# Kernel tuning notes

Measured on AMD Instinct MI355X. Metric: run time of the kernel, lower is better.

## Reference

```python
import jax, jax.numpy as jnp
import numpy as np

B, N, D, H = 8, 1024, 256, 4  # batch, seq, input_dim==output_dim, heads
EPS = 1e-6


def _ln(h, gamma, beta):
    mu = jnp.mean(h, axis=-1, keepdims=True)
    var = jnp.mean(jnp.square(h - mu), axis=-1, keepdims=True)
    return (h - mu) * jax.lax.rsqrt(var + EPS) * gamma + beta


def setup_inputs() -> dict:
    key = jax.random.key(0)
    ks = jax.random.split(key, 8)
    x = jax.random.normal(ks[0], (B, N, D), dtype=jnp.float32)
    mask = jax.random.randint(ks[1], (B, N), 0, 2, dtype=jnp.int32)
    wq = jax.random.normal(ks[2], (H, D, D), dtype=jnp.float32) * 0.05
    wk = jax.random.normal(ks[3], (H, D, D), dtype=jnp.float32) * 0.05
    wv = jax.random.normal(ks[4], (H, D, D), dtype=jnp.float32) * 0.05
    wg = jax.random.uniform(ks[5], (H, D, D), dtype=jnp.float32, minval=-0.05, maxval=0.05)
    out_w = jax.random.normal(ks[6], (D * H, D), dtype=jnp.float32) * 0.05
    out_b = jnp.zeros((D,), dtype=jnp.float32)
    ln_g = jnp.ones((D,), jnp.float32); ln_b = jnp.zeros((D,), jnp.float32)
    lnr_g = jnp.ones((D,), jnp.float32); lnr_b = jnp.zeros((D,), jnp.float32)
    lno_g = jnp.ones((D,), jnp.float32); lno_b = jnp.zeros((D,), jnp.float32)
    return dict(x=x, mask=mask, wq=wq, wk=wk, wv=wv, wg=wg, out_w=out_w, out_b=out_b,
                ln_g=ln_g, ln_b=ln_b, lnr_g=lnr_g, lnr_b=lnr_b, lno_g=lno_g, lno_b=lno_b)


def reference(x, mask, wq, wk, wv, wg, out_w, out_b, ln_g, ln_b, lnr_g, lnr_b, lno_g, lno_b):
    m = mask.astype(jnp.float32)              # (B,N)
    scale = 1.0 / jnp.sqrt(jnp.float32(D))
    x_norm = _ln(x, ln_g, ln_b)               # (B,N,D)
    q = jnp.einsum('bnd,hde->hbne', x_norm, wq)
    k = jnp.einsum('bmd,hde->hbme', x_norm, wk)
    v = jnp.einsum('bmd,hde->hbme', x_norm, wv)
    att = jnp.einsum('hbne,hbme->hbnm', q, k) * scale  # (H,B,N,N)
    amask = m[:, :, None] * m[:, None, :]              # (B,N,N) outer-product mask
    att = att + (1.0 - amask)[None] * (-1e9)           # additive mask
    att = jax.nn.softmax(att, axis=-1) * amask[None]   # multiplicative mask
    out = jnp.einsum('hbnm,hbme->hbne', att, v)        # (H,B,N,D)
    gate = jax.nn.sigmoid(jnp.einsum('bnd,hde->hbne', x_norm, wg))
    out = out * gate
    out = out + x[None]                                # resnet per head
    out = _ln(out, lnr_g, lnr_b)
    out = jnp.transpose(out, (1, 2, 3, 0)).reshape(x.shape[0], x.shape[1], D * H)
    out = out @ out_w + out_b                          # (B,N,D)
    out = out + x                                      # resnet
    out = _ln(out, lno_g, lno_b)
    out = out * m[..., None]
    return out
```

## Files before the change

kernel.cpp:

```cpp
#include <hip/hip_runtime.h>
#include <hip/hip_bf16.h>

#define Bb 8
#define Nn 1024
#define Dd 256
#define Hh 4
#define ROWS 8192
#define EPSf 1e-6f

typedef __bf16 bf16t;
typedef bf16t bf16x8 __attribute__((ext_vector_type(8)));
typedef float f32x4 __attribute__((ext_vector_type(4)));

#define MFMA(a, b, c) __builtin_amdgcn_mfma_f32_16x16x32_bf16((a), (b), (c), 0, 0, 0)
#define GLB_U32(p) ((const __attribute__((address_space(1))) unsigned int*)(p))
#define LDS_U32(p) ((__attribute__((address_space(3))) unsigned int*)(p))

__device__ __forceinline__ bf16x8 load8(const bf16t* p) { return *(const bf16x8*)p; }

__device__ __forceinline__ float ldin(const void* p, size_t i, int flag) {
  return flag ? (float)((const bf16t*)p)[i] : ((const float*)p)[i];
}

__global__ void k_detect(const unsigned int* __restrict__ xw, int* __restrict__ flag) {
  int lane = threadIdx.x;
  int cnt = 0;
  for (int i = lane; i < 4096; i += 64) {
    unsigned int b1 = (xw[i] >> 8) & 0x7F;
    if (b1 >= 0x3B && b1 <= 0x43) cnt++;
  }
#pragma unroll
  for (int off = 32; off > 0; off >>= 1) cnt += __shfl_xor(cnt, off);
  if (lane == 0) *flag = (cnt > 2048) ? 1 : 0;
}

__global__ void k_prep(const void* p0, const void* p1, const void* p2, const void* p3,
                       const void* p4, const void* p5, const void* p6,
                       float* __restrict__ pf, const int* __restrict__ flagp) {
  int flag = *flagp;
  const void* ps[7] = {p0, p1, p2, p3, p4, p5, p6};
  int j = blockIdx.x, i = threadIdx.x;
  pf[j * 256 + i] = ldin(ps[j], i, flag);
}

__global__ __launch_bounds__(256) void k_ln(const void* __restrict__ x,
                                            const float* __restrict__ pf,
                                            bf16t* __restrict__ xn,
                                            float* __restrict__ xf,
                                            const int* __restrict__ flagp) {
  int flag = *flagp;
  int row = blockIdx.x * 4 + (threadIdx.x >> 6);
  int lane = threadIdx.x & 63;
  size_t base = (size_t)row * Dd;
  float v[4]; float s = 0.f, s2 = 0.f;
#pragma unroll
  for (int i = 0; i < 4; ++i) {
    v[i] = ldin(x, base + lane * 4 + i, flag);
    s += v[i]; s2 += v[i] * v[i];
  }
#pragma unroll
  for (int off = 32; off > 0; off >>= 1) {
    s += __shfl_xor(s, off);
    s2 += __shfl_xor(s2, off);
  }
  float mu = s * (1.f / Dd);
  float var = fmaxf(s2 * (1.f / Dd) - mu * mu, 0.f);
  float rs = rsqrtf(var + EPSf);
#pragma unroll
  for (int i = 0; i < 4; ++i) {
    int d = lane * 4 + i;
    xf[base + d] = v[i];
    xn[base + d] = (bf16t)((v[i] - mu) * rs * pf[d] + pf[256 + d]);
  }
}

__global__ __launch_bounds__(256) void k_trall(
    const void* __restrict__ wq, const void* __restrict__ wk,
    const void* __restrict__ wv, const void* __restrict__ wg,
    const void* __restrict__ ow, bf16t* __restrict__ wtAll,
    bf16t* __restrict__ owT, const int* __restrict__ flagp) {
  int flag = *flagp;
  __shared__ bf16t tile[32][33];
  int t = blockIdx.x;
  const void* in; bf16t* out; int R, C; size_t ibase;
  int r0, c0;
  if (t < 1024) {
    int w = t >> 8, z = (t >> 6) & 3, t64 = t & 63;
    r0 = (t64 >> 3) * 32; c0 = (t64 & 7) * 32;
    const void* srcs[4] = {wq, wk, wv, wg};
    const int tslot[4] = {0, 1, 3, 2};
    in = srcs[w]; ibase = (size_t)z * 65536;
    out = wtAll + (size_t)(tslot[w] * 4 + z) * 65536;
    R = 256; C = 256;
  } else {
    int t2 = t - 1024;
    c0 = (t2 & 7) * 32; r0 = (t2 >> 3) * 32;
    in = ow; ibase = 0; out = owT; R = 1024; C = 256;
  }
  int tx = threadIdx.x & 31, ty = threadIdx.x >> 5;
#pragma unroll
  for (int i = 0; i < 32; i += 8)
    tile[ty + i][tx] = (bf16t)ldin(in, ibase + (size_t)(r0 + ty + i) * C + c0 + tx, flag);
  __syncthreads();
#pragma unroll
  for (int i = 0; i < 32; i += 8)
    out[(size_t)(c0 + ty + i) * R + r0 + tx] = tile[tx][ty + i];
}

__global__ __launch_bounds__(256) void k_qkvg(
    const bf16t* __restrict__ xn, const bf16t* __restrict__ wtAll,
    bf16t* __restrict__ q, bf16t* __restrict__ kk,
    bf16t* __restrict__ g, bf16t* __restrict__ vt) {
  const int wave = threadIdx.x >> 6, lane = threadIdx.x & 63;
  const int quad = lane >> 4, l16 = lane & 15;
  const int mi = blockIdx.x, ni = blockIdx.y;
  const int row0 = mi * 128;
  const int instw = ni >> 1, colIn = (ni & 1) * 128;
  const int tt = instw >> 2, h = instw & 3;
  const int rB = (wave >> 1) * 64, cB = (wave & 1) * 64;

  const bf16t* Bsrc = wtAll + (size_t)instw * 65536 + (size_t)colIn * 256;

  __shared__ bf16t aT[4096];
  __shared__ bf16t bT[4096];
  __shared__ bf16t ct[128 * 136];

  f32x4 acc[4][4];
#pragma unroll
  for (int i = 0; i < 4; ++i)
#pragma unroll
    for (int j = 0; j < 4; ++j) acc[i][j] = (f32x4){0.f, 0.f, 0.f, 0.f};

  for (int k0 = 0; k0 < 256; k0 += 32) {
#pragma unroll
    for (int ii = 0; ii < 2; ++ii) {
      int inst = wave * 2 + ii;
      int idx = inst * 64 + lane;
      int r = idx >> 2, cp = idx & 3;
      int c = cp ^ ((r >> 1) & 3);
      __builtin_amdgcn_global_load_lds(GLB_U32(xn + (size_t)(row0 + r) * 256 + k0 + c * 8),
                                       LDS_U32(aT + inst * 512), 16, 0, 0);
    }
#pragma unroll
    for (int ii = 0; ii < 2; ++ii) {
      int inst = wave * 2 + ii;
      int idx = inst * 64 + lane;
      int r = idx >> 2, cp = idx & 3;
      int c = cp ^ ((r >> 1) & 3);
      __builtin_amdgcn_global_load_lds(GLB_U32(Bsrc + (size_t)r * 256 + k0 + c * 8),
                                       LDS_U32(bT + inst * 512), 16, 0, 0);
    }
    __syncthreads();

    bf16x8 aF[4], bF[4];
#pragma unroll
    for (int i = 0; i < 4; ++i) {
      int r = rB + i * 16 + l16;
      aF[i] = *(const bf16x8*)&aT[(r * 4 + (quad ^ ((r >> 1) & 3))) * 8];
    }
#pragma unroll
    for (int j = 0; j < 4; ++j) {
      int r = cB + j * 16 + l16;
      bF[j] = *(const bf16x8*)&bT[(r * 4 + (quad ^ ((r >> 1) & 3))) * 8];
    }
#pragma unroll
    for (int i = 0; i < 4; ++i)
#pragma unroll
      for (int j = 0; j < 4; ++j)
        acc[i][j] = MFMA(aF[i], bF[j], acc[i][j]);
    __syncthreads();
  }

  const bool tr = (tt == 3);
#pragma unroll
  for (int i = 0; i < 4; ++i)
#pragma unroll
    for (int j = 0; j < 4; ++j)
#pragma unroll
      for (int r = 0; r < 4; ++r) {
        int rl = rB + i * 16 + quad * 4 + r, cl = cB + j * 16 + l16;
        if (tr) ct[cl * 136 + rl] = (bf16t)acc[i][j][r];
        else    ct[rl * 136 + cl] = (bf16t)acc[i][j][r];
      }
  __syncthreads();
  if (!tr) {
    bf16t* base = (tt == 0 ? q : (tt == 1 ? kk : g)) +
                  (size_t)h * ROWS * Dd + (size_t)row0 * Dd + colIn;
#pragma unroll
    for (int it = 0; it < 8; ++it) {
      int rl = it * 16 + (threadIdx.x >> 4), c8 = (threadIdx.x & 15) * 8;
      *(bf16x8*)(base + (size_t)rl * Dd + c8) = *(const bf16x8*)&ct[rl * 136 + c8];
    }
  } else {
    int bb = row0 >> 10, n0 = row0 & 1023;
    bf16t* base = vt + (size_t)(h * Bb + bb) * Dd * Nn + (size_t)colIn * Nn + n0;
#pragma unroll
    for (int it = 0; it < 8; ++it) {
      int el = it * 16 + (threadIdx.x >> 4), c8 = (threadIdx.x & 15) * 8;
      *(bf16x8*)(base + (size_t)el * Nn + c8) = *(const bf16x8*)&ct[el * 136 + c8];
    }
  }
}

__global__ __launch_bounds__(256) void k_flash(
    const bf16t* __restrict__ qb, const bf16t* __restrict__ kb,
    const bf16t* __restrict__ vtb, const bf16t* __restrict__ gb,
    const float* __restrict__ xf, const int* __restrict__ mask,
    const float* __restrict__ pf, bf16t* __restrict__ tout) {
  const int wave = threadIdx.x >> 6, lane = threadIdx.x & 63;
  const int quad = lane >> 4, l16 = lane & 15;
  const int lin = blockIdx.x + 16 * blockIdx.y + 128 * blockIdx.z;
  const int hbp = lin & 31, tile = lin >> 5;
  const int b = hbp & 7, h = hbp >> 3;
  const int qrow0 = tile * 64 + wave * 16;

  const bf16t* Q = qb + (size_t)hbp * Nn * Dd;
  const bf16t* K = kb + (size_t)hbp * Nn * Dd;
  const bf16t* V = vtb + (size_t)hbp * Dd * Nn;
  const bf16t* G = gb + (size_t)hbp * Nn * Dd;

  __shared__ bf16t klds[32 * 256];
  __shared__ bf16t vlds[2][256 * 32];
  __shared__ bf16t pl[4 * 16 * 32];
  __shared__ float cm[Nn];

#define SWZ(row_) (((row_) & 3) ^ (((row_) >> 2) & 3))
#define STAGE_K(kt_) do {                                                      \
    _Pragma("unroll") for (int i_ = 0; i_ < 4; ++i_) {                         \
      int inst_ = wave * 4 + i_; int qq_ = inst_ * 64 + lane;                  \
      int r_ = qq_ >> 5, cp_ = qq_ & 31; int c_ = cp_ ^ (r_ & 15);             \
      __builtin_amdgcn_global_load_lds(                                        \
          GLB_U32(K + (size_t)((kt_) + r_) * Dd + c_ * 8),                     \
          LDS_U32(klds + inst_ * 512), 16, 0, 0); } } while (0)
#define STAGE_V(kt_, buf_) do {                                                \
    _Pragma("unroll") for (int i_ = 0; i_ < 4; ++i_) {                         \
      int inst_ = wave * 4 + i_; int qq_ = inst_ * 64 + lane;                  \
      int r_ = qq_ >> 2, cp_ = qq_ & 3; int c_ = cp_ ^ SWZ(r_);                \
      __builtin_amdgcn_global_load_lds(                                        \
          GLB_U32(V + (size_t)r_ * Nn + (kt_) + c_ * 8),                       \
          LDS_U32(vlds[buf_] + inst_ * 512), 16, 0, 0); } } while (0)

  STAGE_V(0, 0);
  STAGE_K(0);
  for (int i = threadIdx.x; i < Nn; i += 256) cm[i] = (float)mask[b * Nn + i];

  bf16x8 aq[8];
#pragma unroll
  for (int k8 = 0; k8 < 8; ++k8)
    aq[k8] = load8(Q + (size_t)(qrow0 + l16) * Dd + k8 * 32 + quad * 8);

  f32x4 oacc[16];
#pragma unroll
  for (int j = 0; j < 16; ++j) oacc[j] = (f32x4){0.f, 0.f, 0.f, 0.f};
  float lpart[4] = {0.f, 0.f, 0.f, 0.f};

  const float scale = 0.0625f;

  for (int kt = 0; kt < Nn; kt += 32) {
    const int vcur = (kt >> 5) & 1;
    __syncthreads();
    if (kt + 32 < Nn) STAGE_V(kt + 32, vcur ^ 1);

    f32x4 sacc[2];
    sacc[0] = (f32x4){0.f, 0.f, 0.f, 0.f};
    sacc[1] = (f32x4){0.f, 0.f, 0.f, 0.f};
#pragma unroll
    for (int k8 = 0; k8 < 8; ++k8)
#pragma unroll
      for (int j = 0; j < 2; ++j) {
        bf16x8 bk = *(const bf16x8*)&klds[((j * 16 + l16) * 32 + ((k8 * 4 + quad) ^ l16)) * 8];
        sacc[j] = MFMA(aq[k8], bk, sacc[j]);
      }

    float cmv0 = cm[kt + l16], cmv1 = cm[kt + 16 + l16];
#pragma unroll
    for (int j = 0; j < 2; ++j) {
      float cmv = j ? cmv1 : cmv0;
#pragma unroll
      for (int r = 0; r < 4; ++r) {
        float e = (cmv != 0.f) ? __expf(sacc[j][r] * scale) : 0.f;
        lpart[r] += e;
        int prow = quad * 4 + r;
        pl[wave * 512 + (prow * 4 + ((j * 2 + (l16 >> 3)) ^ SWZ(prow))) * 8 + (l16 & 7)] = (bf16t)e;
      }
    }

    __builtin_amdgcn_s_barrier();
    if (kt + 32 < Nn) STAGE_K(kt + 32);

    bf16x8 ap = *(const bf16x8*)&pl[wave * 512 + (l16 * 4 + (quad ^ SWZ(l16))) * 8];
#pragma unroll
    for (int j = 0; j < 16; ++j) {
      int e = j * 16 + l16;
      bf16x8 bv = *(const bf16x8*)&vlds[vcur][(e * 4 + (quad ^ SWZ(e))) * 8];
      oacc[j] = MFMA(ap, bv, oacc[j]);
    }
  }

#pragma unroll
  for (int r = 0; r < 4; ++r)
#pragma unroll
    for (int off = 1; off < 16; off <<= 1)
      lpart[r] += __shfl_xor(lpart[r], off);

  float inv[4];
#pragma unroll
  for (int r = 0; r < 4; ++r) {
    float rmv = cm[qrow0 + quad * 4 + r];
    inv[r] = (rmv != 0.f && lpart[r] > 1e-20f) ? 1.f / lpart[r] : 0.f;
  }
  float ps[4] = {0.f, 0.f, 0.f, 0.f}, pq[4] = {0.f, 0.f, 0.f, 0.f};
#pragma unroll
  for (int j = 0; j < 16; ++j) {
    int e = j * 16 + l16;
#pragma unroll
    for (int r = 0; r < 4; ++r) {
      int n = qrow0 + quad * 4 + r;
      float gv = (float)G[(size_t)n * Dd + e];
      float xv = xf[(size_t)(b * Nn + n) * Dd + e];
      float o = oacc[j][r] * inv[r] * (1.f / (1.f + __expf(-gv))) + xv;
      oacc[j][r] = o;
      ps[r] += o; pq[r] += o * o;
    }
  }
#pragma unroll
  for (int r = 0; r < 4; ++r) {
#pragma unroll
    for (int off = 1; off < 16; off <<= 1) {
      ps[r] += __shfl_xor(ps[r], off);
      pq[r] += __shfl_xor(pq[r], off);
    }
    float mu = ps[r] * (1.f / Dd);
    float rs = rsqrtf(fmaxf(pq[r] * (1.f / Dd) - mu * mu, 0.f) + EPSf);
    ps[r] = mu; pq[r] = rs;
  }
#pragma unroll
  for (int j = 0; j < 16; ++j) {
    int e = j * 16 + l16;
    float lg = pf[2 * 256 + e], lb = pf[3 * 256 + e];
#pragma unroll
    for (int r = 0; r < 4; ++r) {
      int n = qrow0 + quad * 4 + r;
      tout[((size_t)(b * Nn + n) * Dd + e) * Hh + h] =
          (bf16t)((oacc[j][r] - ps[r]) * pq[r] * lg + lb);
    }
  }
#undef STAGE_K
#undef STAGE_V
#undef SWZ
}

__global__ __launch_bounds__(256) void k_out(
    const bf16t* __restrict__ t, const bf16t* __restrict__ owT,
    const float* __restrict__ xf, const int* __restrict__ mask,
    const float* __restrict__ pf, void* __restrict__ outp,
    const int* __restrict__ flagp) {
  const int flag = *flagp;
  const int wave = threadIdx.x >> 6, lane = threadIdx.x & 63;
  const int quad = lane >> 4, l16 = lane & 15;
  const int row0 = blockIdx.x * 16;

  f32x4 acc[4];
#pragma unroll
  for (int j = 0; j < 4; ++j) acc[j] = (f32x4){0.f, 0.f, 0.f, 0.f};
  for (int k0 = 0; k0 < 1024; k0 += 32) {
    bf16x8 a = load8(t + (size_t)(row0 + l16) * 1024 + k0 + quad * 8);
#pragma unroll
    for (int j = 0; j < 4; ++j) {
      bf16x8 bb = load8(owT + (size_t)(wave * 64 + j * 16 + l16) * 1024 + k0 + quad * 8);
      acc[j] = MFMA(a, bb, acc[j]);
    }
  }
  __shared__ float redS[4][16], redQ[4][16];
  float ps[4] = {0.f, 0.f, 0.f, 0.f}, pq[4] = {0.f, 0.f, 0.f, 0.f};
#pragma unroll
  for (int j = 0; j < 4; ++j) {
    int e = wave * 64 + j * 16 + l16;
    float bias = pf[6 * 256 + e];
#pragma unroll
    for (int r = 0; r < 4; ++r) {
      int rr = row0 + quad * 4 + r;
      float o = acc[j][r] + bias + xf[(size_t)rr * Dd + e];
      acc[j][r] = o;
      ps[r] += o; pq[r] += o * o;
    }
  }
#pragma unroll
  for (int r = 0; r < 4; ++r) {
#pragma unroll
    for (int off = 1; off < 16; off <<= 1) {
      ps[r] += __shfl_xor(ps[r], off);
      pq[r] += __shfl_xor(pq[r], off);
    }
    if (l16 == 0) { redS[wave][quad * 4 + r] = ps[r]; redQ[wave][quad * 4 + r] = pq[r]; }
  }
  __syncthreads();
  float mu[4], rs[4], mk[4];
#pragma unroll
  for (int r = 0; r < 4; ++r) {
    int rl = quad * 4 + r;
    float ts = redS[0][rl] + redS[1][rl] + redS[2][rl] + redS[3][rl];
    float tq = redQ[0][rl] + redQ[1][rl] + redQ[2][rl] + redQ[3][rl];
    float m_ = ts * (1.f / Dd);
    mu[r] = m_;
    rs[r] = rsqrtf(fmaxf(tq * (1.f / Dd) - m_ * m_, 0.f) + EPSf);
    mk[r] = (float)mask[row0 + rl];
  }
#pragma unroll
  for (int j = 0; j < 4; ++j) {
    int e = wave * 64 + j * 16 + l16;
    float lg = pf[4 * 256 + e], lb = pf[5 * 256 + e];
#pragma unroll
    for (int r = 0; r < 4; ++r) {
      int rr = row0 + quad * 4 + r;
      float o = ((acc[j][r] - mu[r]) * rs[r] * lg + lb) * mk[r];
      size_t idx = (size_t)rr * Dd + e;
      if (flag) ((bf16t*)outp)[idx] = (bf16t)o;
      else      ((float*)outp)[idx] = o;
    }
  }
}

extern "C" void kernel_launch(void* const* d_in, const int* in_sizes, int n_in,
                              void* d_out, int out_size, void* d_ws, size_t ws_size,
                              hipStream_t stream) {
  const void* x    = d_in[0];
  const int*  mask = (const int*)d_in[1];
  const void* wq   = d_in[2];
  const void* wk   = d_in[3];
  const void* wv   = d_in[4];
  const void* wg   = d_in[5];
  const void* ow   = d_in[6];
  const void* ob   = d_in[7];
  const void* lng  = d_in[8];
  const void* lnb  = d_in[9];
  const void* lnrg = d_in[10];
  const void* lnrb = d_in[11];
  const void* lnog = d_in[12];
  const void* lnob = d_in[13];

  char* w = (char*)d_ws;
  int*   flag  = (int*)w;
  float* pf    = (float*)(w + 256);
  w += 8192;
  float* xf    = (float*)w; w += (size_t)ROWS * Dd * 4;
  bf16t* xn    = (bf16t*)w; w += (size_t)ROWS * Dd * 2;
  bf16t* wtAll = (bf16t*)w; w += (size_t)16 * Dd * Dd * 2;
  bf16t* owT   = (bf16t*)w; w += (size_t)Dd * 1024 * 2;
  bf16t* tb    = (bf16t*)w; w += (size_t)ROWS * 1024 * 2;
  bf16t* qb    = (bf16t*)w; w += (size_t)Hh * ROWS * Dd * 2;
  bf16t* kb    = (bf16t*)w; w += (size_t)Hh * ROWS * Dd * 2;
  bf16t* gb    = (bf16t*)w; w += (size_t)Hh * ROWS * Dd * 2;
  bf16t* vtb   = (bf16t*)w; w += (size_t)Hh * ROWS * Dd * 2;

  dim3 blk(256);
  k_detect<<<dim3(1), dim3(64), 0, stream>>>((const unsigned int*)x, flag);
  k_prep<<<dim3(7), blk, 0, stream>>>(lng, lnb, lnrg, lnrb, lnog, lnob, ob, pf, flag);
  k_ln<<<dim3(ROWS / 4), blk, 0, stream>>>(x, pf, xn, xf, flag);
  k_trall<<<dim3(1280), blk, 0, stream>>>(wq, wk, wv, wg, ow, wtAll, owT, flag);
  k_qkvg<<<dim3(64, 32), blk, 0, stream>>>(xn, wtAll, qb, kb, gb, vtb);
  k_flash<<<dim3(16, 8, 4), blk, 0, stream>>>(qb, kb, vtb, gb, xf, mask, pf, tb);
  k_out<<<dim3(512), blk, 0, stream>>>(tb, owT, xf, mask, pf, d_out, flag);
}
```

Measured before the change: 243.2 us.

## Fuse prep kernels into one launch, drop xf copy, stage k_out GEMM via LDS

Merges the dtype-detect, parameter-prep, input layernorm and weight-transpose kernels into a single block-partitioned launch, with each block re-detecting the dtype flag locally from a smaller sample. Stops materializing an fp32 copy of x; the flash and output kernels read the original input through the dtype-aware loader instead. k_out now stages its A and B tiles into swizzled LDS with async global-to-LDS loads rather than loading them per lane from global memory. This removes launch overhead and one full-size write, at the cost of redundant per-block detection and extra barriers in the output GEMM loop.

```diff
diff --git a/kernel.cpp b/kernel.cpp
--- a/kernel.cpp
+++ b/kernel.cpp
@@ -22,89 +22,93 @@
   return flag ? (float)((const bf16t*)p)[i] : ((const float*)p)[i];
 }
 
-__global__ void k_detect(const unsigned int* __restrict__ xw, int* __restrict__ flag) {
-  int lane = threadIdx.x;
-  int cnt = 0;
-  for (int i = lane; i < 4096; i += 64) {
-    unsigned int b1 = (xw[i] >> 8) & 0x7F;
-    if (b1 >= 0x3B && b1 <= 0x43) cnt++;
-  }
-#pragma unroll
-  for (int off = 32; off > 0; off >>= 1) cnt += __shfl_xor(cnt, off);
-  if (lane == 0) *flag = (cnt > 2048) ? 1 : 0;
-}
-
-__global__ void k_prep(const void* p0, const void* p1, const void* p2, const void* p3,
-                       const void* p4, const void* p5, const void* p6,
-                       float* __restrict__ pf, const int* __restrict__ flagp) {
-  int flag = *flagp;
-  const void* ps[7] = {p0, p1, p2, p3, p4, p5, p6};
-  int j = blockIdx.x, i = threadIdx.x;
-  pf[j * 256 + i] = ldin(ps[j], i, flag);
-}
-
-__global__ __launch_bounds__(256) void k_ln(const void* __restrict__ x,
-                                            const float* __restrict__ pf,
-                                            bf16t* __restrict__ xn,
-                                            float* __restrict__ xf,
-                                            const int* __restrict__ flagp) {
-  int flag = *flagp;
-  int row = blockIdx.x * 4 + (threadIdx.x >> 6);
-  int lane = threadIdx.x & 63;
-  size_t base = (size_t)row * Dd;
-  float v[4]; float s = 0.f, s2 = 0.f;
-#pragma unroll
-  for (int i = 0; i < 4; ++i) {
-    v[i] = ldin(x, base + lane * 4 + i, flag);
-    s += v[i]; s2 += v[i] * v[i];
-  }
-#pragma unroll
-  for (int off = 32; off > 0; off >>= 1) {
-    s += __shfl_xor(s, off);
-    s2 += __shfl_xor(s2, off);
-  }
-  float mu = s * (1.f / Dd);
-  float var = fmaxf(s2 * (1.f / Dd) - mu * mu, 0.f);
-  float rs = rsqrtf(var + EPSf);
-#pragma unroll
-  for (int i = 0; i < 4; ++i) {
-    int d = lane * 4 + i;
-    xf[base + d] = v[i];
-    xn[base + d] = (bf16t)((v[i] - mu) * rs * pf[d] + pf[256 + d]);
-  }
-}
-
-__global__ __launch_bounds__(256) void k_trall(
+__global__ __launch_bounds__(256) void k_prepall(
+    const void* __restrict__ x,
     const void* __restrict__ wq, const void* __restrict__ wk,
     const void* __restrict__ wv, const void* __restrict__ wg,
-    const void* __restrict__ ow, bf16t* __restrict__ wtAll,
-    bf16t* __restrict__ owT, const int* __restrict__ flagp) {
-  int flag = *flagp;
-  __shared__ bf16t tile[32][33];
-  int t = blockIdx.x;
-  const void* in; bf16t* out; int R, C; size_t ibase;
-  int r0, c0;
-  if (t < 1024) {
-    int w = t >> 8, z = (t >> 6) & 3, t64 = t & 63;
-    r0 = (t64 >> 3) * 32; c0 = (t64 & 7) * 32;
-    const void* srcs[4] = {wq, wk, wv, wg};
-    const int tslot[4] = {0, 1, 3, 2};
-    in = srcs[w]; ibase = (size_t)z * 65536;
-    out = wtAll + (size_t)(tslot[w] * 4 + z) * 65536;
-    R = 256; C = 256;
+    const void* __restrict__ ow,
+    const void* __restrict__ lng, const void* __restrict__ lnb,
+    const void* __restrict__ lnrg, const void* __restrict__ lnrb,
+    const void* __restrict__ lnog, const void* __restrict__ lnob,
+    const void* __restrict__ ob,
+    bf16t* __restrict__ xn, bf16t* __restrict__ wtAll,
+    bf16t* __restrict__ owT, float* __restrict__ pf, int* __restrict__ flagOut) {
+  __shared__ int sflag;
+  {
+    if (threadIdx.x < 64) {
+      int lane = threadIdx.x;
+      int cnt = 0;
+      const unsigned int* xw = (const unsigned int*)x;
+#pragma unroll
+      for (int i = 0; i < 4; ++i) {
+        unsigned int b1 = (xw[lane * 4 + i] >> 8) & 0x7F;
+        if (b1 >= 0x3B && b1 <= 0x43) cnt++;
+      }
+#pragma unroll
+      for (int off = 32; off > 0; off >>= 1) cnt += __shfl_xor(cnt, off);
+      if (lane == 0) sflag = (cnt > 128) ? 1 : 0;
+    }
+    __syncthreads();
+  }
+  const int flag = sflag;
+  const int bid = blockIdx.x;
+
+  if (bid < 2048) {
+    int row = bid * 4 + (threadIdx.x >> 6);
+    int lane = threadIdx.x & 63;
+    size_t base = (size_t)row * Dd;
+    float v[4]; float s = 0.f, s2 = 0.f;
+#pragma unroll
+    for (int i = 0; i < 4; ++i) {
+      v[i] = ldin(x, base + lane * 4 + i, flag);
+      s += v[i]; s2 += v[i] * v[i];
+    }
+#pragma unroll
+    for (int off = 32; off > 0; off >>= 1) {
+      s += __shfl_xor(s, off);
+      s2 += __shfl_xor(s2, off);
+    }
+    float mu = s * (1.f / Dd);
+    float var = fmaxf(s2 * (1.f / Dd) - mu * mu, 0.f);
+    float rs = rsqrtf(var + EPSf);
+#pragma unroll
+    for (int i = 0; i < 4; ++i) {
+      int d = lane * 4 + i;
+      xn[base + d] = (bf16t)((v[i] - mu) * rs * ldin(lng, d, flag) + ldin(lnb, d, flag));
+    }
+  } else if (bid < 3328) {
+    __shared__ bf16t tile[32][33];
+    int t = bid - 2048;
+    const void* in; bf16t* out; int R, C; size_t ibase;
+    int r0, c0;
+    if (t < 1024) {
+      int w = t >> 8, z = (t >> 6) & 3, t64 = t & 63;
+      r0 = (t64 >> 3) * 32; c0 = (t64 & 7) * 32;
+      const void* srcs[4] = {wq, wk, wv, wg};
+      const int tslot[4] = {0, 1, 3, 2};
+      in = srcs[w]; ibase = (size_t)z * 65536;
+      out = wtAll + (size_t)(tslot[w] * 4 + z) * 65536;
+      R = 256; C = 256;
+    } else {
+      int t2 = t - 1024;
+      c0 = (t2 & 7) * 32; r0 = (t2 >> 3) * 32;
+      in = ow; ibase = 0; out = owT; R = 1024; C = 256;
+    }
+    int tx = threadIdx.x & 31, ty = threadIdx.x >> 5;
+#pragma unroll
+    for (int i = 0; i < 32; i += 8)
+      tile[ty + i][tx] = (bf16t)ldin(in, ibase + (size_t)(r0 + ty + i) * C + c0 + tx, flag);
+    __syncthreads();
+#pragma unroll
+    for (int i = 0; i < 32; i += 8)
+      out[(size_t)(c0 + ty + i) * R + r0 + tx] = tile[tx][ty + i];
   } else {
-    int t2 = t - 1024;
-    c0 = (t2 & 7) * 32; r0 = (t2 >> 3) * 32;
-    in = ow; ibase = 0; out = owT; R = 1024; C = 256;
-  }
-  int tx = threadIdx.x & 31, ty = threadIdx.x >> 5;
-#pragma unroll
-  for (int i = 0; i < 32; i += 8)
-    tile[ty + i][tx] = (bf16t)ldin(in, ibase + (size_t)(r0 + ty + i) * C + c0 + tx, flag);
-  __syncthreads();
-#pragma unroll
-  for (int i = 0; i < 32; i += 8)
-    out[(size_t)(c0 + ty + i) * R + r0 + tx] = tile[tx][ty + i];
+    const void* ps[7] = {lng, lnb, lnrg, lnrb, lnog, lnob, ob};
+#pragma unroll
+    for (int j = 0; j < 7; ++j)
+      pf[j * 256 + threadIdx.x] = ldin(ps[j], threadIdx.x, flag);
+    if (threadIdx.x == 0) *flagOut = flag;
+  }
 }
 
 __global__ __launch_bounds__(256) void k_qkvg(
@@ -205,8 +209,10 @@
 __global__ __launch_bounds__(256) void k_flash(
     const bf16t* __restrict__ qb, const bf16t* __restrict__ kb,
     const bf16t* __restrict__ vtb, const bf16t* __restrict__ gb,
-    const float* __restrict__ xf, const int* __restrict__ mask,
-    const float* __restrict__ pf, bf16t* __restrict__ tout) {
+    const void* __restrict__ xin, const int* __restrict__ mask,
+    const float* __restrict__ pf, const int* __restrict__ flagp,
+    bf16t* __restrict__ tout) {
+  const int flag = *flagp;
   const int wave = threadIdx.x >> 6, lane = threadIdx.x & 63;
   const int quad = lane >> 4, l16 = lane & 15;
   const int lin = blockIdx.x + 16 * blockIdx.y + 128 * blockIdx.z;
@@ -317,7 +323,7 @@
     for (int r = 0; r < 4; ++r) {
       int n = qrow0 + quad * 4 + r;
       float gv = (float)G[(size_t)n * Dd + e];
-      float xv = xf[(size_t)(b * Nn + n) * Dd + e];
+      float xv = ldin(xin, (size_t)(b * Nn + n) * Dd + e, flag);
       float o = oacc[j][r] * inv[r] * (1.f / (1.f + __expf(-gv))) + xv;
       oacc[j][r] = o;
       ps[r] += o; pq[r] += o * o;
@@ -352,7 +358,7 @@
 
 __global__ __launch_bounds__(256) void k_out(
     const bf16t* __restrict__ t, const bf16t* __restrict__ owT,
-    const float* __restrict__ xf, const int* __restrict__ mask,
+    const void* __restrict__ xin, const int* __restrict__ mask,
     const float* __restrict__ pf, void* __restrict__ outp,
     const int* __restrict__ flagp) {
   const int flag = *flagp;
@@ -360,18 +366,41 @@
   const int quad = lane >> 4, l16 = lane & 15;
   const int row0 = blockIdx.x * 16;
 
+  __shared__ bf16t aT[512];
+  __shared__ bf16t bT[8192];
+  __shared__ float redS[4][16], redQ[4][16];
+
   f32x4 acc[4];
 #pragma unroll
   for (int j = 0; j < 4; ++j) acc[j] = (f32x4){0.f, 0.f, 0.f, 0.f};
+
   for (int k0 = 0; k0 < 1024; k0 += 32) {
-    bf16x8 a = load8(t + (size_t)(row0 + l16) * 1024 + k0 + quad * 8);
+    if (wave == 0) {
+      int r = lane >> 2, cp = lane & 3;
+      int c = cp ^ ((r >> 1) & 3);
+      __builtin_amdgcn_global_load_lds(GLB_U32(t + (size_t)(row0 + r) * 1024 + k0 + c * 8),
+                                       LDS_U32(aT), 16, 0, 0);
+    }
+#pragma unroll
+    for (int ii = 0; ii < 4; ++ii) {
+      int inst = wave * 4 + ii;
+      int idx = inst * 64 + lane;
+      int r = idx >> 2, cp = idx & 3;
+      int c = cp ^ ((r >> 1) & 3);
+      __builtin_amdgcn_global_load_lds(GLB_U32(owT + (size_t)r * 1024 + k0 + c * 8),
+                                       LDS_U32(bT + inst * 512), 16, 0, 0);
+    }
+    __syncthreads();
+    bf16x8 a = *(const bf16x8*)&aT[(l16 * 4 + (quad ^ ((l16 >> 1) & 3))) * 8];
 #pragma unroll
     for (int j = 0; j < 4; ++j) {
-      bf16x8 bb = load8(owT + (size_t)(wave * 64 + j * 16 + l16) * 1024 + k0 + quad * 8);
+      int r = wave * 64 + j * 16 + l16;
+      bf16x8 bb = *(const bf16x8*)&bT[(r * 4 + (quad ^ ((r >> 1) & 3))) * 8];
       acc[j] = MFMA(a, bb, acc[j]);
     }
-  }
-  __shared__ float redS[4][16], redQ[4][16];
+    __syncthreads();
+  }
+
   float ps[4] = {0.f, 0.f, 0.f, 0.f}, pq[4] = {0.f, 0.f, 0.f, 0.f};
 #pragma unroll
   for (int j = 0; j < 4; ++j) {
@@ -380,7 +409,7 @@
 #pragma unroll
     for (int r = 0; r < 4; ++r) {
       int rr = row0 + quad * 4 + r;
-      float o = acc[j][r] + bias + xf[(size_t)rr * Dd + e];
+      float o = acc[j][r] + bias + ldin(xin, (size_t)rr * Dd + e, flag);
       acc[j][r] = o;
       ps[r] += o; pq[r] += o * o;
     }
@@ -443,7 +472,6 @@
   int*   flag  = (int*)w;
   float* pf    = (float*)(w + 256);
   w += 8192;
-  float* xf    = (float*)w; w += (size_t)ROWS * Dd * 4;
   bf16t* xn    = (bf16t*)w; w += (size_t)ROWS * Dd * 2;
   bf16t* wtAll = (bf16t*)w; w += (size_t)16 * Dd * Dd * 2;
   bf16t* owT   = (bf16t*)w; w += (size_t)Dd * 1024 * 2;
@@ -454,11 +482,10 @@
   bf16t* vtb   = (bf16t*)w; w += (size_t)Hh * ROWS * Dd * 2;
 
   dim3 blk(256);
-  k_detect<<<dim3(1), dim3(64), 0, stream>>>((const unsigned int*)x, flag);
-  k_prep<<<dim3(7), blk, 0, stream>>>(lng, lnb, lnrg, lnrb, lnog, lnob, ob, pf, flag);
-  k_ln<<<dim3(ROWS / 4), blk, 0, stream>>>(x, pf, xn, xf, flag);
-  k_trall<<<dim3(1280), blk, 0, stream>>>(wq, wk, wv, wg, ow, wtAll, owT, flag);
+  k_prepall<<<dim3(3329), blk, 0, stream>>>(x, wq, wk, wv, wg, ow,
+                                            lng, lnb, lnrg, lnrb, lnog, lnob, ob,
+                                            xn, wtAll, owT, pf, flag);
   k_qkvg<<<dim3(64, 32), blk, 0, stream>>>(xn, wtAll, qb, kb, gb, vtb);
-  k_flash<<<dim3(16, 8, 4), blk, 0, stream>>>(qb, kb, vtb, gb, xf, mask, pf, tb);
-  k_out<<<dim3(512), blk, 0, stream>>>(tb, owT, xf, mask, pf, d_out, flag);
-}
+  k_flash<<<dim3(16, 8, 4), blk, 0, stream>>>(qb, kb, vtb, gb, x, mask, pf, flag, tb);
+  k_out<<<dim3(512), blk, 0, stream>>>(tb, owT, x, mask, pf, d_out, flag);
+}
```

Measured after the change: 251.3 us. +3.4%, slower.
